# Optimization experiments

Measured on AMD Instinct MI355X. Metric: run time of the kernel, lower is better.

## Reference

```python
import jax, jax.numpy as jnp
import numpy as np
from jax import lax

NUM_AGNN_LAYERS = 32  # module stacks hidden_dim AGNNConv layers
EPS = 1e-12           # F.normalize clamp


def setup_inputs() -> dict:
    key = jax.random.key(0)
    k1, k2, k3, k4 = jax.random.split(key, 4)
    N, F_in, H, C, E = 100000, 512, 32, 40, 3200000
    x = jax.random.normal(k1, (N, F_in), dtype=jnp.float32)
    edge_index = jax.random.randint(k2, (2, E), 0, N, dtype=jnp.int64)
    W1 = jax.random.normal(k3, (F_in, H), dtype=jnp.float32) * (1.0 / np.sqrt(F_in))
    b1 = jnp.zeros((H,), dtype=jnp.float32)
    W2 = jax.random.normal(k4, (H, C), dtype=jnp.float32) * (1.0 / np.sqrt(H))
    b2 = jnp.zeros((C,), dtype=jnp.float32)
    return {"x": x, "edge_index": edge_index, "W1": W1, "b1": b1, "W2": W2, "b2": b2}


def reference(x, edge_index, W1, b1, W2, b2):
    N = x.shape[0]
    loops = jnp.arange(N, dtype=edge_index.dtype)
    src = jnp.concatenate([edge_index[0], loops])  # message source j
    dst = jnp.concatenate([edge_index[1], loops])  # message target i (softmax group)

    def agnn(h, _):
        # cosine attention, beta = 1 (requires_grad=False)
        norm = jnp.maximum(jnp.linalg.norm(h, axis=-1, keepdims=True), EPS)
        hn = h / norm
        alpha = jnp.sum(hn[src] * hn[dst], axis=-1)               # [E+N]
        m = jax.ops.segment_max(alpha, dst, num_segments=N)       # stable softmax
        e = jnp.exp(alpha - m[dst])
        s = jax.ops.segment_sum(e, dst, num_segments=N)
        coef = e / s[dst]
        out = jax.ops.segment_sum(h[src] * coef[:, None], dst, num_segments=N)
        return out, None

    h = jax.nn.relu(x @ W1 + b1)
    h, _ = lax.scan(agnn, h, None, length=NUM_AGNN_LAYERS)
    logits = h @ W2 + b2
    return jax.nn.log_softmax(logits, axis=1)
```

## Files before the change

kernel.cpp:

```cpp
#include <hip/hip_runtime.h>
#include <math.h>


#define HDIM 32
#define NBMAX 1024
#define BSH 7
#define CHUNK 32768

typedef _Float16 f16;
typedef _Float16 v2h __attribute__((ext_vector_type(2)));
typedef _Float16 f16x8 __attribute__((ext_vector_type(8)));
typedef float f32x4 __attribute__((ext_vector_type(4)));

struct __attribute__((aligned(16))) H8 { v2h p[4]; };
struct __attribute__((aligned(8)))  H4 { v2h p[2]; };

#if defined(__has_builtin)
#if __has_builtin(__builtin_amdgcn_fdot2)
#define FDOT2(a, b, c) __builtin_amdgcn_fdot2((a), (b), (c), false)
#endif
#if __has_builtin(__builtin_amdgcn_update_dpp)
#define HAS_DPP 1
#endif
#endif
#ifndef FDOT2
#define FDOT2(a, b, c) fmaf((float)(a)[1], (float)(b)[1], fmaf((float)(a)[0], (float)(b)[0], (c)))
#endif

static __device__ __forceinline__ float quad_sum(float x) {
#ifdef HAS_DPP
    x += __int_as_float(__builtin_amdgcn_update_dpp(
        0, __float_as_int(x), 0xB1 , 0xF, 0xF, true));
    x += __int_as_float(__builtin_amdgcn_update_dpp(
        0, __float_as_int(x), 0x4E , 0xF, 0xF, true));
#else
    x += __shfl_xor(x, 1);
    x += __shfl_xor(x, 2);
#endif
    return x;
}

static __device__ __forceinline__ int eread(const int* __restrict__ e, int i64, long long idx) {
    return i64 ? e[2 * idx] : e[idx];
}

__global__ void k_flag(const int* __restrict__ e, int* __restrict__ flag) {
    if (blockIdx.x == 0 && threadIdx.x == 0) {
        int z = 0;
        for (int k = 0; k < 64; ++k) z |= e[2 * k + 1];
        *flag = (z == 0) ? 1 : 0;
    }
}

__global__ void k_zero(int* __restrict__ p, int n) {
    int i = blockIdx.x * blockDim.x + threadIdx.x;
    if (i < n) p[i] = 0;
}

__launch_bounds__(256) __global__
void k_hist(const int* __restrict__ e, const int* __restrict__ flag,
            int* __restrict__ gc, int* __restrict__ blockOffs,
            long long E, long long M) {
    __shared__ int bh[NBMAX];
    for (int t = threadIdx.x; t < NBMAX; t += 256) bh[t] = 0;
    __syncthreads();
    int i64 = *flag;
    long long base = (long long)blockIdx.x * CHUNK;
    long long end = base + CHUNK < M ? base + CHUNK : M;
    for (long long m = base + threadIdx.x; m < end; m += 256) {
        int d = (m < E) ? eread(e, i64, E + m) : (int)(m - E);
        atomicAdd(&bh[d >> BSH], 1);
    }
    __syncthreads();
    for (int t = threadIdx.x; t < NBMAX; t += 256) {
        int c = bh[t];
        int off = 0;
        if (c) off = atomicAdd(&gc[t], c);
        blockOffs[(size_t)blockIdx.x * NBMAX + t] = off;
    }
}

__launch_bounds__(256) __global__
void k_bscan(const int* __restrict__ gc, int* __restrict__ bbase,
             int* __restrict__ rp, int N) {
    __shared__ int lds[256];
    int t = threadIdx.x;
    int v[4];
#pragma unroll
    for (int d = 0; d < 4; ++d) v[d] = gc[t * 4 + d];
    int tsum = v[0] + v[1] + v[2] + v[3];
    lds[t] = tsum;
    __syncthreads();
    int acc = tsum;
    for (int sh = 1; sh < 256; sh <<= 1) {
        int x = (t >= sh) ? lds[t - sh] : 0;
        __syncthreads();
        acc += x;
        lds[t] = acc;
        __syncthreads();
    }
    if (t == 255) { rp[N] = acc; bbase[NBMAX] = acc; }
    int run = acc - tsum;
#pragma unroll
    for (int d = 0; d < 4; ++d) { bbase[t * 4 + d] = run; run += v[d]; }
}

__launch_bounds__(256) __global__
void k_part(const int* __restrict__ e, const int* __restrict__ flag,
            const int* __restrict__ bbase, const int* __restrict__ blockOffs,
            int2* __restrict__ pair, long long E, long long M) {
    __shared__ int cur[NBMAX];
    for (int t = threadIdx.x; t < NBMAX; t += 256)
        cur[t] = bbase[t] + blockOffs[(size_t)blockIdx.x * NBMAX + t];
    __syncthreads();
    int i64 = *flag;
    long long base = (long long)blockIdx.x * CHUNK;
    long long end = base + CHUNK < M ? base + CHUNK : M;
    for (long long m = base + threadIdx.x; m < end; m += 256) {
        int s, d;
        if (m < E) { s = eread(e, i64, m); d = eread(e, i64, E + m); }
        else { s = d = (int)(m - E); }
        int pos = atomicAdd(&cur[d >> BSH], 1);
        pair[pos] = make_int2(s, d);
    }
}

__launch_bounds__(256) __global__
void k_fine(const int2* __restrict__ pair, const int* __restrict__ bbase,
            int* __restrict__ rp, int* __restrict__ col, int N) {
    __shared__ int cnt[128];
    __shared__ int sc[128];
    int b = blockIdx.x;
    int beg = bbase[b];
    int end = bbase[b + 1];
    int t = threadIdx.x;
    if (t < 128) cnt[t] = 0;
    __syncthreads();
    for (int k = beg + t; k < end; k += 256)
        atomicAdd(&cnt[pair[k].y & 127], 1);
    __syncthreads();
    if (t < 128) sc[t] = cnt[t];
    __syncthreads();
    for (int sh = 1; sh < 128; sh <<= 1) {
        int x = 0;
        if (t < 128 && t >= sh) x = sc[t - sh];
        __syncthreads();
        if (t < 128) sc[t] += x;
        __syncthreads();
    }
    if (t < 128) {
        int basepos = beg + sc[t] - cnt[t];
        int d = (b << BSH) + t;
        if (d < N) rp[d] = basepos;
        cnt[t] = basepos;
    }
    __syncthreads();
    for (int k = beg + t; k < end; k += 256) {
        int2 p = pair[k];
        int pos = atomicAdd(&cnt[p.y & 127], 1);
        col[pos] = p.x;
    }
}

__global__ void k_w1cvt(const float* __restrict__ W1, f16* __restrict__ W1hT) {
    int t = blockIdx.x * 256 + threadIdx.x;
    if (t < 512 * 32) {
        int k = t >> 5, j = t & 31;
        W1hT[(size_t)j * 512 + k] = (f16)W1[t];
    }
}

__launch_bounds__(256) __global__
void k_gemm1(const float* __restrict__ x, const f16* __restrict__ W1hT,
             const float* __restrict__ b1, f16* __restrict__ h,
             float* __restrict__ invn, int N) {
    int wid = (blockIdx.x * 256 + threadIdx.x) >> 6;
    int lane = threadIdx.x & 63;
    int ntile = (N + 15) >> 4;
    if (wid >= ntile) return;
    int j16 = lane & 15;
    int kb = lane >> 4;
    int rload = wid * 16 + j16;
    if (rload > N - 1) rload = N - 1;
    const float* xr = x + (size_t)rload * 512 + kb * 8;
    const f16* w0 = W1hT + (size_t)j16 * 512 + kb * 8;
    const f16* w1 = W1hT + (size_t)(j16 + 16) * 512 + kb * 8;
    f32x4 acc0 = {0.f, 0.f, 0.f, 0.f};
    f32x4 acc1 = {0.f, 0.f, 0.f, 0.f};
#pragma unroll 4
    for (int ks = 0; ks < 16; ++ks) {
        float4 xa = *(const float4*)(xr + ks * 32);
        float4 xb = *(const float4*)(xr + ks * 32 + 4);
        f16x8 a;
        a[0] = (f16)xa.x; a[1] = (f16)xa.y; a[2] = (f16)xa.z; a[3] = (f16)xa.w;
        a[4] = (f16)xb.x; a[5] = (f16)xb.y; a[6] = (f16)xb.z; a[7] = (f16)xb.w;
        f16x8 b0 = *(const f16x8*)(w0 + ks * 32);
        f16x8 b1v = *(const f16x8*)(w1 + ks * 32);
        acc0 = __builtin_amdgcn_mfma_f32_16x16x32_f16(a, b0, acc0, 0, 0, 0);
        acc1 = __builtin_amdgcn_mfma_f32_16x16x32_f16(a, b1v, acc1, 0, 0, 0);
    }
    float bias0 = b1[j16];
    float bias1 = b1[j16 + 16];
#pragma unroll
    for (int r = 0; r < 4; ++r) {
        float v0 = fmaxf(acc0[r] + bias0, 0.0f);
        float v1 = fmaxf(acc1[r] + bias1, 0.0f);
        float ss = fmaf(v0, v0, v1 * v1);
        ss += __shfl_xor(ss, 1);
        ss += __shfl_xor(ss, 2);
        ss += __shfl_xor(ss, 4);
        ss += __shfl_xor(ss, 8);
        int row = wid * 16 + 4 * kb + r;
        if (row < N) {
            h[(size_t)row * HDIM + j16] = (f16)v0;
            h[(size_t)row * HDIM + j16 + 16] = (f16)v1;
            if (j16 == 0) invn[row] = 1.0f / fmaxf(sqrtf(ss), 1e-12f);
        }
    }
}

__launch_bounds__(256) __global__
void k_agnn(const f16* __restrict__ h_in, const float* __restrict__ inv_in,
            f16* __restrict__ h_out, float* __restrict__ inv_out,
            const int* __restrict__ rp, const int* __restrict__ col, int N) {
    int wave = threadIdx.x >> 6;
    int lane = threadIdx.x & 63;
    int i = blockIdx.x * 4 + wave;
    if (i >= N) return;
    int beg = rp[i];
    int deg = rp[i + 1] - beg;
    int eloc = lane >> 2;
    int c8 = lane & 3;
    float inv_i = inv_in[i];
    H8 hi = *(const H8*)(h_in + (size_t)i * HDIM + 8 * c8);
    float s_run = 0.0f;
    float acc[8] = {0.f, 0.f, 0.f, 0.f, 0.f, 0.f, 0.f, 0.f};
    int nchunk = (deg + 15) >> 4;
    int cv = (lane < deg) ? col[beg + lane] : 0;
    H8 rA, rB;
    float iA, iB = 0.0f;
    bool vA, vB = false;
    {
        vA = eloc < deg;
        int s = __shfl(cv, eloc);
        s = vA ? s : 0;
        rA = *(const H8*)(h_in + (size_t)s * HDIM + 8 * c8);
        iA = inv_in[s];
    }
    if (nchunk > 1) {
        int idx = 16 + eloc;
        vB = idx < deg;
        int s = __shfl(cv, 16 | eloc);
        s = vB ? s : 0;
        rB = *(const H8*)(h_in + (size_t)s * HDIM + 8 * c8);
        iB = inv_in[s];
    } else {
        rB = hi;
    }
    for (int ck = 0; ck < nchunk; ++ck) {
        H8 rc = rA;
        float ic = iA;
        bool vc = vA;
        rA = rB; iA = iB; vA = vB;
        int nc = ck + 2;
        if (nc < nchunk) {
            if ((nc & 3) == 0) {
                int idx64 = nc * 16 + lane;
                cv = (idx64 < deg) ? col[beg + idx64] : 0;
            }
            int idx = nc * 16 + eloc;
            vB = idx < deg;
            int s = __shfl(cv, ((nc & 3) << 4) | eloc);
            s = vB ? s : 0;
            rB = *(const H8*)(h_in + (size_t)s * HDIM + 8 * c8);
            iB = inv_in[s];
        }
        float dot = 0.0f;
#pragma unroll
        for (int j = 0; j < 4; ++j) dot = FDOT2(rc.p[j], hi.p[j], dot);
        dot = quad_sum(dot);
        float e = vc ? __expf(fmaf(dot, inv_i * ic, -1.0f)) : 0.0f;
        s_run += e;
#pragma unroll
        for (int j = 0; j < 4; ++j) {
            acc[2 * j + 0] = fmaf(e, (float)rc.p[j][0], acc[2 * j + 0]);
            acc[2 * j + 1] = fmaf(e, (float)rc.p[j][1], acc[2 * j + 1]);
        }
    }
    float s_tot = s_run;
#pragma unroll
    for (int mask = 4; mask <= 32; mask <<= 1) s_tot += __shfl_xor(s_tot, mask);
#pragma unroll
    for (int mask = 4; mask <= 32; mask <<= 1) {
#pragma unroll
        for (int j = 0; j < 8; ++j) acc[j] += __shfl_xor(acc[j], mask);
    }
    float invs = 1.0f / s_tot;
    float ss = 0.0f;
#pragma unroll
    for (int j = 0; j < 8; ++j) {
        acc[j] *= invs;
        ss = fmaf(acc[j], acc[j], ss);
    }
    ss = quad_sum(ss);
    if (lane < 4) {
        H8 o;
#pragma unroll
        for (int j = 0; j < 4; ++j) {
            o.p[j][0] = (f16)acc[2 * j + 0];
            o.p[j][1] = (f16)acc[2 * j + 1];
        }
        *(H8*)(h_out + (size_t)i * HDIM + 8 * lane) = o;
        if (lane == 0) inv_out[i] = 1.0f / fmaxf(sqrtf(ss), 1e-12f);
    }
}

__launch_bounds__(256) __global__
void k_gemm2(const f16* __restrict__ h, const float* __restrict__ W2,
             const float* __restrict__ b2, float* __restrict__ out, int N) {
    int wave = threadIdx.x >> 6;
    int lane = threadIdx.x & 63;
    int i = blockIdx.x * 4 + wave;
    if (i >= N) return;
    bool act = lane < 40;
    float acc = act ? b2[lane] : 0.0f;
    const f16* hr = h + (size_t)i * HDIM;
#pragma unroll
    for (int k = 0; k < HDIM; ++k) {
        float hk = (float)hr[k];
        float w = act ? W2[k * 40 + lane] : 0.0f;
        acc = fmaf(hk, w, acc);
    }
    float logit = act ? acc : -INFINITY;
    float m = logit;
#pragma unroll
    for (int mask = 32; mask >= 1; mask >>= 1) m = fmaxf(m, __shfl_xor(m, mask));
    float e = act ? __expf(logit - m) : 0.0f;
    float s = e;
#pragma unroll
    for (int mask = 32; mask >= 1; mask >>= 1) s += __shfl_xor(s, mask);
    float res = logit - m - __logf(s);
    if (act) out[(size_t)i * 40 + lane] = res;
}

extern "C" void kernel_launch(void* const* d_in, const int* in_sizes, int n_in,
                              void* d_out, int out_size, void* d_ws, size_t ws_size,
                              hipStream_t stream) {
    const float* x  = (const float*)d_in[0];
    const int*   e  = (const int*)d_in[1];
    const float* W1 = (const float*)d_in[2];
    const float* b1 = (const float*)d_in[3];
    const float* W2 = (const float*)d_in[4];
    const float* b2 = (const float*)d_in[5];
    float* out = (float*)d_out;

    const long long E = (long long)in_sizes[1] / 2;
    const int N = in_sizes[0] / 512;
    const long long M = E + N;
    const int nblk = (int)((M + CHUNK - 1) / CHUNK);

    char* w = (char*)d_ws;
    auto alloc = [&](size_t bytes) -> void* {
        void* p = (void*)w;
        w += (bytes + 255) & ~(size_t)255;
        return p;
    };
    int*  flag      = (int*)alloc(4);
    int*  gc        = (int*)alloc(NBMAX * 4);
    int*  bbase     = (int*)alloc((NBMAX + 1) * 4);
    int*  blockOffs = (int*)alloc((size_t)nblk * NBMAX * 4);
    int2* pair      = (int2*)alloc((size_t)M * 8);
    int*  rp        = (int*)alloc(((size_t)N + 1) * 4);
    int*  col       = (int*)alloc((size_t)M * 4);
    f16*  hA   = (f16*)alloc((size_t)N * HDIM * 2);
    f16*  hB   = (f16*)alloc((size_t)N * HDIM * 2);
    float* invA = (float*)alloc((size_t)N * 4);
    float* invB = (float*)alloc((size_t)N * 4);
    f16*  W1hT = (f16*)alloc((size_t)512 * 32 * 2);
    if ((size_t)(w - (char*)d_ws) > ws_size) return;

    k_flag<<<1, 64, 0, stream>>>(e, flag);
    k_zero<<<(NBMAX + 255) / 256, 256, 0, stream>>>(gc, NBMAX);
    k_hist<<<nblk, 256, 0, stream>>>(e, flag, gc, blockOffs, E, M);
    k_bscan<<<1, 256, 0, stream>>>(gc, bbase, rp, N);
    k_part<<<nblk, 256, 0, stream>>>(e, flag, bbase, blockOffs, pair, E, M);
    k_fine<<<NBMAX, 256, 0, stream>>>(pair, bbase, rp, col, N);

    k_w1cvt<<<64, 256, 0, stream>>>(W1, W1hT);
    int ntile = (N + 15) >> 4;
    k_gemm1<<<(ntile + 3) / 4, 256, 0, stream>>>(x, W1hT, b1, hA, invA, N);

    f16 *hin = hA, *hout = hB;
    float *iin = invA, *iout = invB;
    for (int l = 0; l < 32; ++l) {
        k_agnn<<<(N + 3) / 4, 256, 0, stream>>>(hin, iin, hout, iout, rp, col, N);
        f16* t = hin; hin = hout; hout = t;
        float* ti = iin; iin = iout; iout = ti;
    }
    k_gemm2<<<(N + 3) / 4, 256, 0, stream>>>(hin, W2, b2, out, N);
}
```

Before: 2.097 ms.

## Split AGNN gather into two source-half passes for cache locality

Each node's neighbor list is partitioned by whether the source index falls in the lower or upper half of nodes, and each layer runs two passes. Each pass gathers only from one half of h, and partial sums and accumulators go through a scratch buffer between passes. The aim is to keep the gathered working set in L2/MALL for better hit rates. In exchange it doubles the kernel launches, adds per-node partial-accumulator traffic and extra index reads, and includes a one-time split kernel. Nontemporal loads and stores are also used for indices and partials.

```diff
diff --git a/kernel.cpp b/kernel.cpp
--- a/kernel.cpp
+++ b/kernel.cpp
@@ -13,7 +13,6 @@
 typedef float f32x4 __attribute__((ext_vector_type(4)));
 
 struct __attribute__((aligned(16))) H8 { v2h p[4]; };
-struct __attribute__((aligned(8)))  H4 { v2h p[2]; };
 
 #if defined(__has_builtin)
 #if __has_builtin(__builtin_amdgcn_fdot2)
@@ -159,6 +158,22 @@
         int2 p = pair[k];
         int pos = atomicAdd(&cnt[p.y & 127], 1);
         col[pos] = p.x;
+    }
+}
+
+__launch_bounds__(256) __global__
+void k_split(const int* __restrict__ rp, const int* __restrict__ col,
+             int* __restrict__ colS, int* __restrict__ mid, int N, int half) {
+    int i = blockIdx.x * 256 + threadIdx.x;
+    if (i >= N) return;
+    int beg = rp[i], end = rp[i + 1];
+    int c = 0;
+    for (int k = beg; k < end; ++k) c += (col[k] < half) ? 1 : 0;
+    int a = beg, b = beg + c;
+    mid[i] = b;
+    for (int k = beg; k < end; ++k) {
+        int s = col[k];
+        if (s < half) colS[a++] = s; else colS[b++] = s;
     }
 }
 
@@ -222,21 +237,33 @@
 __launch_bounds__(256) __global__
 void k_agnn(const f16* __restrict__ h_in, const float* __restrict__ inv_in,
             f16* __restrict__ h_out, float* __restrict__ inv_out,
-            const int* __restrict__ rp, const int* __restrict__ col, int N) {
+            const int* __restrict__ rp, const int* __restrict__ mid,
+            const int* __restrict__ colS,
+            float* __restrict__ sp, float* __restrict__ accP,
+            int N, int pass) {
     int wave = threadIdx.x >> 6;
     int lane = threadIdx.x & 63;
     int i = blockIdx.x * 4 + wave;
     if (i >= N) return;
-    int beg = rp[i];
-    int deg = rp[i + 1] - beg;
+    int beg = pass ? mid[i] : rp[i];
+    int end = pass ? rp[i + 1] : mid[i];
+    int deg = end - beg;
     int eloc = lane >> 2;
     int c8 = lane & 3;
     float inv_i = inv_in[i];
     H8 hi = *(const H8*)(h_in + (size_t)i * HDIM + 8 * c8);
     float s_run = 0.0f;
     float acc[8] = {0.f, 0.f, 0.f, 0.f, 0.f, 0.f, 0.f, 0.f};
+    if (pass && lane < 4) {
+        const f32x4* ap = (const f32x4*)(accP + (size_t)i * 32 + lane * 8);
+        f32x4 p0 = __builtin_nontemporal_load(ap);
+        f32x4 p1 = __builtin_nontemporal_load(ap + 1);
+        acc[0] = p0[0]; acc[1] = p0[1]; acc[2] = p0[2]; acc[3] = p0[3];
+        acc[4] = p1[0]; acc[5] = p1[1]; acc[6] = p1[2]; acc[7] = p1[3];
+        s_run = __builtin_nontemporal_load(sp + i);
+    }
     int nchunk = (deg + 15) >> 4;
-    int cv = (lane < deg) ? col[beg + lane] : 0;
+    int cv = (lane < deg) ? __builtin_nontemporal_load(colS + beg + lane) : 0;
     H8 rA, rB;
     float iA, iB = 0.0f;
     bool vA, vB = false;
@@ -266,7 +293,7 @@
         if (nc < nchunk) {
             if ((nc & 3) == 0) {
                 int idx64 = nc * 16 + lane;
-                cv = (idx64 < deg) ? col[beg + idx64] : 0;
+                cv = (idx64 < deg) ? __builtin_nontemporal_load(colS + beg + idx64) : 0;
             }
             int idx = nc * 16 + eloc;
             vB = idx < deg;
@@ -294,6 +321,17 @@
     for (int mask = 4; mask <= 32; mask <<= 1) {
 #pragma unroll
         for (int j = 0; j < 8; ++j) acc[j] += __shfl_xor(acc[j], mask);
+    }
+    if (!pass) {
+        if (lane < 4) {
+            f32x4 q0 = {acc[0], acc[1], acc[2], acc[3]};
+            f32x4 q1 = {acc[4], acc[5], acc[6], acc[7]};
+            f32x4* ap = (f32x4*)(accP + (size_t)i * 32 + lane * 8);
+            __builtin_nontemporal_store(q0, ap);
+            __builtin_nontemporal_store(q1, ap + 1);
+            if (lane == 0) __builtin_nontemporal_store(s_tot, sp + i);
+        }
+        return;
     }
     float invs = 1.0f / s_tot;
     float ss = 0.0f;
@@ -372,6 +410,7 @@
     int2* pair      = (int2*)alloc((size_t)M * 8);
     int*  rp        = (int*)alloc(((size_t)N + 1) * 4);
     int*  col       = (int*)alloc((size_t)M * 4);
+    int*  mid       = (int*)alloc((size_t)N * 4);
     f16*  hA   = (f16*)alloc((size_t)N * HDIM * 2);
     f16*  hB   = (f16*)alloc((size_t)N * HDIM * 2);
     float* invA = (float*)alloc((size_t)N * 4);
@@ -379,12 +418,29 @@
     f16*  W1hT = (f16*)alloc((size_t)512 * 32 * 2);
     if ((size_t)(w - (char*)d_ws) > ws_size) return;
 
+    float* sp; int* colS; float* accP;
+    {
+        size_t need = (size_t)N * 4 + (size_t)M * 4 + (size_t)N * 128;
+        char* pb = (char*)pair;
+        if (need <= (size_t)M * 8) {
+            sp   = (float*)pb;
+            colS = (int*)(pb + (size_t)N * 4);
+            accP = (float*)(pb + (size_t)N * 4 + (size_t)M * 4);
+        } else {
+            sp   = (float*)alloc((size_t)N * 4);
+            colS = (int*)alloc((size_t)M * 4);
+            accP = (float*)alloc((size_t)N * 128);
+            if ((size_t)(w - (char*)d_ws) > ws_size) return;
+        }
+    }
+
     k_flag<<<1, 64, 0, stream>>>(e, flag);
     k_zero<<<(NBMAX + 255) / 256, 256, 0, stream>>>(gc, NBMAX);
     k_hist<<<nblk, 256, 0, stream>>>(e, flag, gc, blockOffs, E, M);
     k_bscan<<<1, 256, 0, stream>>>(gc, bbase, rp, N);
     k_part<<<nblk, 256, 0, stream>>>(e, flag, bbase, blockOffs, pair, E, M);
     k_fine<<<NBMAX, 256, 0, stream>>>(pair, bbase, rp, col, N);
+    k_split<<<(N + 255) / 256, 256, 0, stream>>>(rp, col, colS, mid, N, N >> 1);
 
     k_w1cvt<<<64, 256, 0, stream>>>(W1, W1hT);
     int ntile = (N + 15) >> 4;
@@ -393,7 +449,10 @@
     f16 *hin = hA, *hout = hB;
     float *iin = invA, *iout = invB;
     for (int l = 0; l < 32; ++l) {
-        k_agnn<<<(N + 3) / 4, 256, 0, stream>>>(hin, iin, hout, iout, rp, col, N);
+        k_agnn<<<(N + 3) / 4, 256, 0, stream>>>(hin, iin, hout, iout,
+                                                rp, mid, colS, sp, accP, N, 0);
+        k_agnn<<<(N + 3) / 4, 256, 0, stream>>>(hin, iin, hout, iout,
+                                                rp, mid, colS, sp, accP, N, 1);
         f16* t = hin; hin = hout; hout = t;
         float* ti = iin; iin = iout; iout = ti;
     }
```

Measured after the change: 3.467 ms. 1.65x slower.
